# Performance work log

Measured on AMD Instinct MI355X. Metric: run time of the kernel, lower is better.

## Reference

```python
import jax, jax.numpy as jnp
import numpy as np

N_NODES = 51200
N_GRAPHS = 64
NODES_PER_GRAPH = 800
N_EDGES = 819200
DIM_IN = 128
DIM_HIDDEN = 64
HEADS = 3
DIM_OUT = 64


def leaky(x, slope):
    return jnp.where(x >= 0, x, slope * x)


def setup_inputs() -> dict:
    key = jax.random.key(0)
    ks = jax.random.split(key, 12)
    s = lambda fan_in: 1.0 / np.sqrt(fan_in)
    X = jax.random.normal(ks[0], (N_NODES, DIM_IN), dtype=jnp.float32)
    edge_indices = jax.random.randint(ks[1], (2, N_EDGES), 0, N_NODES, dtype=jnp.int32)
    ptr = (jnp.arange(N_GRAPHS + 1, dtype=jnp.int32) * NODES_PER_GRAPH)
    # linearSeq: Linear(dim_in, dim_hidden) + LeakyReLU
    W1 = jax.random.uniform(ks[2], (DIM_IN, DIM_HIDDEN), jnp.float32, -s(DIM_IN), s(DIM_IN))
    b1 = jax.random.uniform(ks[3], (DIM_HIDDEN,), jnp.float32, -s(DIM_IN), s(DIM_IN))
    # GATConv params: lin_src/lin_dst (no bias), att_src/att_dst, bias (concat=False -> out_channels)
    W_src = jax.random.uniform(ks[4], (DIM_HIDDEN, HEADS * DIM_HIDDEN), jnp.float32, -s(DIM_HIDDEN), s(DIM_HIDDEN))
    W_dst = jax.random.uniform(ks[5], (DIM_HIDDEN, HEADS * DIM_HIDDEN), jnp.float32, -s(DIM_HIDDEN), s(DIM_HIDDEN))
    att_src = jax.random.normal(ks[6], (HEADS, DIM_HIDDEN), dtype=jnp.float32) * 0.1
    att_dst = jax.random.normal(ks[7], (HEADS, DIM_HIDDEN), dtype=jnp.float32) * 0.1
    gat_bias = jnp.zeros((DIM_HIDDEN,), dtype=jnp.float32)
    # linear_final: Linear(2*dim_hidden, dim_out)
    Wf = jax.random.uniform(ks[8], (2 * DIM_HIDDEN, DIM_OUT), jnp.float32, -s(2 * DIM_HIDDEN), s(2 * DIM_HIDDEN))
    bf = jax.random.uniform(ks[9], (DIM_OUT,), jnp.float32, -s(2 * DIM_HIDDEN), s(2 * DIM_HIDDEN))
    return {"X": X, "W1": W1, "b1": b1, "W_src": W_src, "W_dst": W_dst,
            "att_src": att_src, "att_dst": att_dst, "gat_bias": gat_bias,
            "Wf": Wf, "bf": bf, "edge_indices": edge_indices, "ptr": ptr}


def reference(X, W1, b1, W_src, W_dst, att_src, att_dst, gat_bias, Wf, bf, edge_indices, ptr):
    N = X.shape[0]
    src, dst = edge_indices[0], edge_indices[1]  # message flows src -> dst
    # input projection
    h = leaky(X @ W1 + b1, 0.01)                                  # [N, DH]
    # GATConv (heads=3, concat=False, add_self_loops=False)
    x_src = (h @ W_src).reshape(N, HEADS, DIM_HIDDEN)             # [N, H, C]
    x_dst = (h @ W_dst).reshape(N, HEADS, DIM_HIDDEN)
    a_src = jnp.einsum('nhc,hc->nh', x_src, att_src)              # [N, H]
    a_dst = jnp.einsum('nhc,hc->nh', x_dst, att_dst)
    logits = leaky(a_src[src] + a_dst[dst], 0.2)                  # [E, H]
    # segment softmax over incoming edges of each target node
    m = jax.ops.segment_max(logits, dst, num_segments=N)          # [N, H]
    e = jnp.exp(logits - m[dst])
    denom = jax.ops.segment_sum(e, dst, num_segments=N)           # [N, H]
    attn = e / denom[dst]                                         # [E, H]
    msg = x_src[src] * attn[..., None]                            # [E, H, C]
    agg = jax.ops.segment_sum(msg, dst, num_segments=N)           # [N, H, C]
    out = agg.mean(axis=1) + gat_bias                             # concat=False -> head mean
    # final head
    cat = jnp.concatenate([h, out], axis=1)                       # [N, 2*DH]
    y = leaky(cat, 0.01) @ Wf + bf                                # [N, DO]
    # aggregate_using_ptr: mean-pool nodes per graph using CSR ptr
    node_graph = jnp.searchsorted(ptr, jnp.arange(N), side='right') - 1
    sums = jax.ops.segment_sum(y, node_graph, num_segments=ptr.shape[0] - 1)
    counts = (ptr[1:] - ptr[:-1]).astype(y.dtype)
    pooled = sums / counts[:, None]                               # [n_graphs, DO]
    return pooled, attn
```

## Files before the change

### kernel.cpp

```cpp
#include <hip/hip_runtime.h>
#include <hip/hip_bf16.h>

#define N_NODES   51200
#define N_GRAPHS  64
#define N_EDGES   819200
#define DIM_IN    128
#define DH        64
#define HEADS     3
#define DIM_OUT   64
#define CAP       96
#define NPART     8
#define PART_SZ   (N_NODES / NPART)

typedef __hip_bfloat16 bf16;
typedef short bf16x8 __attribute__((ext_vector_type(8)));
typedef float f32x4  __attribute__((ext_vector_type(4)));

__device__ __forceinline__ float b2f(bf16 x) { return __bfloat162float(x); }
__device__ __forceinline__ bf16  f2b(float x) { return __float2bfloat16(x); }
__device__ __forceinline__ short f2bs(float x) { return (short)__bfloat16_as_ushort(f2b(x)); }
__device__ __forceinline__ float leaky(float x, float s) { return x >= 0.f ? x : s * x; }
__device__ __forceinline__ float ldin(const void* p, size_t i, int f32) {
    return f32 ? ((const float*)p)[i] : b2f(((const bf16*)p)[i]);
}
__device__ __forceinline__ bf16x8 ld8(const void* p, size_t i, int f32) {
    if (!f32) return *((const bf16x8*)((const short*)p + i));
    const float* f = (const float*)p + i;
    bf16x8 r;
    #pragma unroll
    for (int j = 0; j < 8; ++j) r[j] = f2bs(f[j]);
    return r;
}

__global__ __launch_bounds__(256) void detect_kernel(const unsigned short* __restrict__ Xu,
                                                     int* __restrict__ flag) {
    __shared__ int cnt;
    int tid = threadIdx.x;
    if (tid == 0) cnt = 0;
    __syncthreads();
    int local = 0;
    for (int i = tid * 2; i < 8192; i += 512) {
        unsigned e = (Xu[i] >> 7) & 0xFF;
        if (e >= 110 && e <= 135) local++;
    }
    atomicAdd(&cnt, local);
    __syncthreads();
    if (tid == 0) *flag = (cnt < 2048) ? 1 : 0;
}

__global__ __launch_bounds__(256) void scatter_prep_kernel(const int* __restrict__ src,
                                                           const int* __restrict__ dst,
                                                           int* __restrict__ cursor,
                                                           unsigned short* __restrict__ bucket,
                                                           const void* __restrict__ W1,
                                                           const void* __restrict__ Wsrc,
                                                           const void* __restrict__ Wdst,
                                                           const void* __restrict__ Wf,
                                                           const void* __restrict__ att_src,
                                                           const void* __restrict__ att_dst,
                                                           const int* __restrict__ flagp,
                                                           short* __restrict__ W1t,
                                                           short* __restrict__ Wspt,
                                                           short* __restrict__ Wft,
                                                           short* __restrict__ Wat) {
    if (blockIdx.x < NPART * (N_EDGES / 2048)) {
        const int p = blockIdx.x & (NPART - 1);
        const int slice = blockIdx.x >> 3;
        const int lo = p * PART_SZ, hi = lo + PART_SZ;
        const int base = slice * 2048 + threadIdx.x;
        #pragma unroll
        for (int t = 0; t < 8; ++t) {
            int e = base + t * 256;
            int d = dst[e];
            if (d >= lo && d < hi) {
                int pos = atomicAdd(&cursor[d], 1);
                if (pos < CAP) bucket[(size_t)d * CAP + pos] = (unsigned short)src[e];
            }
        }
        return;
    }
    const int f32 = *flagp;
    int idx = (blockIdx.x - NPART * (N_EDGES / 2048)) * 256 + threadIdx.x;
    if (idx < 8192) {
        int n = idx >> 7, k = idx & 127;
        W1t[idx] = f2bs(ldin(W1, (size_t)k * 64 + n, f32));
    } else if (idx < 20480) {
        int j = idx - 8192;
        int col = j / 192;
        int rem = j - col * 192;
        int h = rem >> 6, kk = rem & 63;
        Wspt[j] = f2bs(ldin(Wsrc, (size_t)kk * 192 + h * 64 + col, f32) * (1.0f / 3.0f));
    } else if (idx < 28672) {
        int j = idx - 20480;
        int n = j >> 7, k = j & 127;
        Wft[j] = f2bs(ldin(Wf, (size_t)k * 64 + n, f32));
    } else if (idx < 29696) {
        int j = idx - 28672;
        int n = j >> 6, k = j & 63;
        float v = 0.f;
        if (n < 3) {
            for (int c = 0; c < 64; ++c)
                v += ldin(Wsrc, (size_t)k * 192 + n * 64 + c, f32) * ldin(att_src, n * 64 + c, f32);
        } else if (n < 6) {
            for (int c = 0; c < 64; ++c)
                v += ldin(Wdst, (size_t)k * 192 + (n - 3) * 64 + c, f32) * ldin(att_dst, (n - 3) * 64 + c, f32);
        }
        Wat[j] = f2bs(v);
    }
}

__global__ __launch_bounds__(256) void k1_kernel(const void* __restrict__ X,
                                                 const short* __restrict__ W1t,
                                                 const short* __restrict__ Wat,
                                                 const void* __restrict__ b1,
                                                 const int* __restrict__ flagp,
                                                 bf16* __restrict__ h_bf,
                                                 float* __restrict__ a_src4,
                                                 float* __restrict__ a_dst4) {
    const int f32 = *flagp;
    __shared__ short hs[64 * 72];
    const int tid  = threadIdx.x;
    const int w    = tid >> 6;
    const int lane = tid & 63;
    const int lm   = lane & 15;
    const int q    = lane >> 4;
    const int row0 = blockIdx.x * 64;

    const float bias = ldin(b1, w * 16 + lm, f32);
    for (int mt = 0; mt < 4; ++mt) {
        f32x4 acc = {0.f, 0.f, 0.f, 0.f};
        #pragma unroll
        for (int kc = 0; kc < 4; ++kc) {
            bf16x8 a = ld8(X, (size_t)(row0 + mt * 16 + lm) * 128 + kc * 32 + q * 8, f32);
            bf16x8 b = *((const bf16x8*)(W1t + (size_t)(w * 16 + lm) * 128 + kc * 32 + q * 8));
            acc = __builtin_amdgcn_mfma_f32_16x16x32_bf16(a, b, acc, 0, 0, 0);
        }
        #pragma unroll
        for (int r = 0; r < 4; ++r) {
            int row = mt * 16 + q * 4 + r;
            float v = leaky(acc[r] + bias, 0.01f);
            short hv = f2bs(v);
            hs[row * 72 + w * 16 + lm] = hv;
            h_bf[(size_t)(row0 + row) * 64 + w * 16 + lm] = __ushort_as_bfloat16((unsigned short)hv);
        }
    }
    __syncthreads();

    {
        const int mt = w;
        bf16x8 a0  = *((const bf16x8*)(hs + (mt * 16 + lm) * 72 + q * 8));
        bf16x8 a1  = *((const bf16x8*)(hs + (mt * 16 + lm) * 72 + 32 + q * 8));
        bf16x8 b0  = *((const bf16x8*)(Wat + (size_t)lm * 64 + q * 8));
        bf16x8 b1v = *((const bf16x8*)(Wat + (size_t)lm * 64 + 32 + q * 8));
        f32x4 acca = {0.f, 0.f, 0.f, 0.f};
        acca = __builtin_amdgcn_mfma_f32_16x16x32_bf16(a0, b0, acca, 0, 0, 0);
        acca = __builtin_amdgcn_mfma_f32_16x16x32_bf16(a1, b1v, acca, 0, 0, 0);
        if (lm < 6) {
            #pragma unroll
            for (int r = 0; r < 4; ++r) {
                int row = row0 + mt * 16 + q * 4 + r;
                if (lm < 3) a_src4[(size_t)row * 4 + lm] = acca[r];
                else        a_dst4[(size_t)row * 4 + (lm - 3)] = acca[r];
            }
        }
    }
}

__global__ __launch_bounds__(256) void edge_kernel(const unsigned short* __restrict__ bucket,
                                                   const int* __restrict__ cursor,
                                                   const float* __restrict__ a_src4,
                                                   const float* __restrict__ a_dst4,
                                                   const unsigned short* __restrict__ hu,
                                                   float4* __restrict__ dstinfo,
                                                   bf16* __restrict__ wagg) {
    const int lane = threadIdx.x & 63;
    const int w = threadIdx.x >> 6;
    const int n = blockIdx.x * 4 + w;
    const int dg = min(cursor[n], CAP);
    const float4 ad = ((const float4*)a_dst4)[n];
    __shared__ float4 buf[4][64];
    float den0 = 0.f, den1 = 0.f, den2 = 0.f;
    float acc0 = 0.f, acc1 = 0.f, acc2 = 0.f;
    for (int c0 = 0; c0 < dg; c0 += 64) {
        int cnt = min(64, dg - c0);
        if (lane < cnt) {
            int s = bucket[n * CAP + c0 + lane];
            const float4 as = ((const float4*)a_src4)[s];
            float e0 = __expf(leaky(as.x + ad.x, 0.2f));
            float e1 = __expf(leaky(as.y + ad.y, 0.2f));
            float e2 = __expf(leaky(as.z + ad.z, 0.2f));
            buf[w][lane] = make_float4(e0, e1, e2, __int_as_float(s));
        }
        asm volatile("s_waitcnt lgkmcnt(0)" ::: "memory");
        int j = 0;
        for (; j + 8 <= cnt; j += 8) {
            float4 r[8]; unsigned short hv[8];
            #pragma unroll
            for (int u = 0; u < 8; ++u) r[u] = buf[w][j + u];
            #pragma unroll
            for (int u = 0; u < 8; ++u)
                hv[u] = hu[(((unsigned)__float_as_int(r[u].w)) << 6) | (unsigned)lane];
            #pragma unroll
            for (int u = 0; u < 8; ++u) {
                float f = b2f(__ushort_as_bfloat16(hv[u]));
                acc0 += r[u].x * f; acc1 += r[u].y * f; acc2 += r[u].z * f;
                den0 += r[u].x;     den1 += r[u].y;     den2 += r[u].z;
            }
        }
        for (; j < cnt; ++j) {
            float4 r = buf[w][j];
            unsigned short hvv = hu[(((unsigned)__float_as_int(r.w)) << 6) | (unsigned)lane];
            float f = b2f(__ushort_as_bfloat16(hvv));
            acc0 += r.x * f; acc1 += r.y * f; acc2 += r.z * f;
            den0 += r.x;     den1 += r.y;     den2 += r.z;
        }
    }
    float inv0 = den0 > 0.f ? 1.f / den0 : 0.f;
    float inv1 = den1 > 0.f ? 1.f / den1 : 0.f;
    float inv2 = den2 > 0.f ? 1.f / den2 : 0.f;
    size_t wb = (size_t)n * 192;
    wagg[wb + lane]       = f2b(acc0 * inv0);
    wagg[wb + 64 + lane]  = f2b(acc1 * inv1);
    wagg[wb + 128 + lane] = f2b(acc2 * inv2);
    if (lane == 0) {
        dstinfo[(size_t)n * 2 + 0] = make_float4(ad.x, ad.y, ad.z, 0.f);
        dstinfo[(size_t)n * 2 + 1] = make_float4(inv0, inv1, inv2, 0.f);
    }
}

__global__ __launch_bounds__(256) void attn_g3_kernel(const int* __restrict__ src,
                                                      const int* __restrict__ dst,
                                                      const float* __restrict__ a_src4,
                                                      const float4* __restrict__ dstinfo,
                                                      const bf16* __restrict__ h_bf,
                                                      const bf16* __restrict__ wagg,
                                                      const short* __restrict__ Wspt,
                                                      const short* __restrict__ Wft,
                                                      const void* __restrict__ gat_bias,
                                                      const void* __restrict__ bfv,
                                                      const int* __restrict__ flagp,
                                                      bf16* __restrict__ y_bf,
                                                      void* __restrict__ d_out) {
    const int f32 = *flagp;
    __shared__ short cs[64 * 136];
    if (blockIdx.x < N_EDGES / 256) {
        int e = blockIdx.x * 256 + threadIdx.x;
        int s = src[e], d = dst[e];
        const float4 as = ((const float4*)a_src4)[s];
        const float4 ad = dstinfo[(size_t)d * 2 + 0];
        const float4 cv = dstinfo[(size_t)d * 2 + 1];
        float a0 = __expf(leaky(as.x + ad.x, 0.2f)) * cv.x;
        float a1 = __expf(leaky(as.y + ad.y, 0.2f)) * cv.y;
        float a2 = __expf(leaky(as.z + ad.z, 0.2f)) * cv.z;
        size_t o = (size_t)N_GRAPHS * DIM_OUT + (size_t)e * 3;
        if (f32) {
            float* p = (float*)d_out;
            p[o] = a0; p[o + 1] = a1; p[o + 2] = a2;
        } else {
            bf16* p = (bf16*)d_out;
            p[o] = f2b(a0); p[o + 1] = f2b(a1); p[o + 2] = f2b(a2);
        }
        return;
    }
    const int bid  = blockIdx.x - N_EDGES / 256;
    const int tid  = threadIdx.x;
    const int w    = tid >> 6;
    const int lane = tid & 63;
    const int lm   = lane & 15;
    const int q    = lane >> 4;
    const int row0 = bid * 64;
    for (int idx = tid; idx < 64 * 64; idx += 256) {
        int r = idx >> 6, k = idx & 63;
        cs[r * 136 + k] = f2bs(leaky(b2f(h_bf[(size_t)(row0 + r) * 64 + k]), 0.01f));
    }
    {
        const int col = w * 16 + lm;
        const float gb = ldin(gat_bias, col, f32);
        for (int mt = 0; mt < 4; ++mt) {
            f32x4 acc = {0.f, 0.f, 0.f, 0.f};
            #pragma unroll
            for (int kc = 0; kc < 6; ++kc) {
                bf16x8 a = *((const bf16x8*)((const short*)wagg + (size_t)(row0 + mt * 16 + lm) * 192 + kc * 32 + q * 8));
                bf16x8 b = *((const bf16x8*)(Wspt + (size_t)col * 192 + kc * 32 + q * 8));
                acc = __builtin_amdgcn_mfma_f32_16x16x32_bf16(a, b, acc, 0, 0, 0);
            }
            #pragma unroll
            for (int r = 0; r < 4; ++r) {
                int row = mt * 16 + q * 4 + r;
                cs[row * 136 + 64 + col] = f2bs(leaky(acc[r] + gb, 0.01f));
            }
        }
    }
    __syncthreads();
    const float bias = ldin(bfv, w * 16 + lm, f32);
    for (int mt = 0; mt < 4; ++mt) {
        f32x4 acc = {0.f, 0.f, 0.f, 0.f};
        #pragma unroll
        for (int kc = 0; kc < 4; ++kc) {
            bf16x8 a = *((const bf16x8*)(cs + (mt * 16 + lm) * 136 + kc * 32 + q * 8));
            bf16x8 b = *((const bf16x8*)(Wft + (size_t)(w * 16 + lm) * 128 + kc * 32 + q * 8));
            acc = __builtin_amdgcn_mfma_f32_16x16x32_bf16(a, b, acc, 0, 0, 0);
        }
        #pragma unroll
        for (int r = 0; r < 4; ++r) {
            int row = row0 + mt * 16 + q * 4 + r;
            y_bf[(size_t)row * 64 + w * 16 + lm] = f2b(acc[r] + bias);
        }
    }
}

__global__ __launch_bounds__(1024) void pool_kernel(const bf16* __restrict__ y_bf,
                                                    const int* __restrict__ ptr,
                                                    const int* __restrict__ flagp,
                                                    void* __restrict__ d_out) {
    __shared__ float part[16][64];
    const int f32 = *flagp;
    const int g = blockIdx.x;
    const int w = threadIdx.x >> 6, lane = threadIdx.x & 63;
    const int lo = ptr[g], hi = ptr[g + 1];
    const int cnt = hi - lo;
    float s = 0.f;
    for (int i = lo + w; i < hi; i += 16) s += b2f(y_bf[(size_t)i * DIM_OUT + lane]);
    part[w][lane] = s;
    __syncthreads();
    if (threadIdx.x < 64) {
        float t = 0.f;
        #pragma unroll
        for (int k = 0; k < 16; ++k) t += part[k][threadIdx.x];
        float v = t / (float)cnt;
        if (f32) ((float*)d_out)[g * DIM_OUT + threadIdx.x] = v;
        else     ((bf16*)d_out)[g * DIM_OUT + threadIdx.x]  = f2b(v);
    }
}

extern "C" void kernel_launch(void* const* d_in, const int* in_sizes, int n_in,
                              void* d_out, int out_size, void* d_ws, size_t ws_size,
                              hipStream_t stream) {
    const void* X        = d_in[0];
    const void* W1       = d_in[1];
    const void* b1       = d_in[2];
    const void* Wsrc     = d_in[3];
    const void* Wdst     = d_in[4];
    const void* att_src  = d_in[5];
    const void* att_dst  = d_in[6];
    const void* gat_bias = d_in[7];
    const void* Wf       = d_in[8];
    const void* bfv      = d_in[9];
    const int*  ei       = (const int*)d_in[10];
    const int*  ptr      = (const int*)d_in[11];
    const int*  src  = ei;
    const int*  dstp = ei + N_EDGES;

    char* ws = (char*)d_ws;
    size_t off_b = 0;
    auto alloc = [&](size_t bytes) -> char* {
        char* p = ws + off_b;
        off_b += (bytes + 255) & ~(size_t)255;
        return p;
    };
    int*     flag    = (int*)    alloc(256);
    short*   W1t     = (short*)  alloc(8192 * 2);
    short*   Wspt    = (short*)  alloc(12288 * 2);
    short*   Wft     = (short*)  alloc(8192 * 2);
    short*   Wat     = (short*)  alloc(1024 * 2);
    bf16*    h_bf    = (bf16*)   alloc((size_t)N_NODES * 64 * 2);
    float*   a_src4  = (float*)  alloc((size_t)N_NODES * 16);
    float*   a_dst4  = (float*)  alloc((size_t)N_NODES * 16);
    float4*  dstinfo = (float4*) alloc((size_t)N_NODES * 2 * 16);
    bf16*    wagg    = (bf16*)   alloc((size_t)N_NODES * 192 * 2);
    int*     cursor  = (int*)    alloc((size_t)N_NODES * 4);
    unsigned short* bucket = (unsigned short*)alloc((size_t)N_NODES * CAP * 2);
    bf16*    y_bf    = (bf16*)   bucket;
    if (off_b > ws_size) return;

    hipLaunchKernelGGL(detect_kernel, dim3(1), dim3(256), 0, stream,
                       (const unsigned short*)X, flag);
    hipMemsetAsync(cursor, 0, (size_t)N_NODES * 4, stream);
    hipLaunchKernelGGL(scatter_prep_kernel,
                       dim3(NPART * (N_EDGES / 2048) + 116), dim3(256), 0, stream,
                       src, dstp, cursor, bucket,
                       W1, Wsrc, Wdst, Wf, att_src, att_dst, flag, W1t, Wspt, Wft, Wat);
    hipLaunchKernelGGL(k1_kernel, dim3(N_NODES / 64), dim3(256), 0, stream,
                       X, W1t, Wat, b1, flag, h_bf, a_src4, a_dst4);
    hipLaunchKernelGGL(edge_kernel, dim3(N_NODES / 4), dim3(256), 0, stream,
                       bucket, cursor, a_src4, a_dst4,
                       (const unsigned short*)h_bf, dstinfo, wagg);
    hipLaunchKernelGGL(attn_g3_kernel, dim3(N_EDGES / 256 + N_NODES / 64), dim3(256), 0, stream,
                       src, dstp, a_src4, dstinfo, h_bf, wagg, Wspt, Wft,
                       gat_bias, bfv, flag, y_bf, d_out);
    hipLaunchKernelGGL(pool_kernel, dim3(N_GRAPHS), dim3(1024), 0, stream, y_bf, ptr, flag, d_out);
}
```

Baseline: 237.5 us.

## Fuse edge scatter with input projection and gather fp8 node features

Splits the weight prep into a small prep kernel for W1/attention vectors, then fuses the edge bucketing scatter, the input projection GEMM, and the remaining weight transposes into a single multi-role kernel so they run concurrently. The projection now also writes an fp8 copy of h, which the edge aggregation kernel gathers instead of bf16 to halve random-gather bytes. The softmax denominator is accumulated once per edge during exp computation and reduced with a wave shuffle instead of being redundantly summed per lane. This trades accuracy of the aggregated messages (fp8 quantisation) for bandwidth, and adds an extra launch plus extra h8 writes.

New measurement: 248.8 us. 1.05x slower.

```diff
diff --git a/kernel.cpp b/kernel.cpp
--- a/kernel.cpp
+++ b/kernel.cpp
@@ -11,6 +11,9 @@
 #define CAP       96
 #define NPART     8
 #define PART_SZ   (N_NODES / NPART)
+#define SC_BLOCKS (NPART * (N_EDGES / 2048))
+#define K1_BLOCKS (N_NODES / 64)
+#define P2_BLOCKS 80
 
 typedef __hip_bfloat16 bf16;
 typedef short bf16x8 __attribute__((ext_vector_type(8)));
@@ -48,54 +51,21 @@
     if (tid == 0) *flag = (cnt < 2048) ? 1 : 0;
 }
 
-__global__ __launch_bounds__(256) void scatter_prep_kernel(const int* __restrict__ src,
-                                                           const int* __restrict__ dst,
-                                                           int* __restrict__ cursor,
-                                                           unsigned short* __restrict__ bucket,
-                                                           const void* __restrict__ W1,
-                                                           const void* __restrict__ Wsrc,
-                                                           const void* __restrict__ Wdst,
-                                                           const void* __restrict__ Wf,
-                                                           const void* __restrict__ att_src,
-                                                           const void* __restrict__ att_dst,
-                                                           const int* __restrict__ flagp,
-                                                           short* __restrict__ W1t,
-                                                           short* __restrict__ Wspt,
-                                                           short* __restrict__ Wft,
-                                                           short* __restrict__ Wat) {
-    if (blockIdx.x < NPART * (N_EDGES / 2048)) {
-        const int p = blockIdx.x & (NPART - 1);
-        const int slice = blockIdx.x >> 3;
-        const int lo = p * PART_SZ, hi = lo + PART_SZ;
-        const int base = slice * 2048 + threadIdx.x;
-        #pragma unroll
-        for (int t = 0; t < 8; ++t) {
-            int e = base + t * 256;
-            int d = dst[e];
-            if (d >= lo && d < hi) {
-                int pos = atomicAdd(&cursor[d], 1);
-                if (pos < CAP) bucket[(size_t)d * CAP + pos] = (unsigned short)src[e];
-            }
-        }
-        return;
-    }
+__global__ __launch_bounds__(256) void prep1_kernel(const void* __restrict__ W1,
+                                                    const void* __restrict__ Wsrc,
+                                                    const void* __restrict__ Wdst,
+                                                    const void* __restrict__ att_src,
+                                                    const void* __restrict__ att_dst,
+                                                    const int* __restrict__ flagp,
+                                                    short* __restrict__ W1t,
+                                                    short* __restrict__ Wat) {
     const int f32 = *flagp;
-    int idx = (blockIdx.x - NPART * (N_EDGES / 2048)) * 256 + threadIdx.x;
+    int idx = blockIdx.x * 256 + threadIdx.x;
     if (idx < 8192) {
         int n = idx >> 7, k = idx & 127;
         W1t[idx] = f2bs(ldin(W1, (size_t)k * 64 + n, f32));
-    } else if (idx < 20480) {
+    } else if (idx < 9216) {
         int j = idx - 8192;
-        int col = j / 192;
-        int rem = j - col * 192;
-        int h = rem >> 6, kk = rem & 63;
-        Wspt[j] = f2bs(ldin(Wsrc, (size_t)kk * 192 + h * 64 + col, f32) * (1.0f / 3.0f));
-    } else if (idx < 28672) {
-        int j = idx - 20480;
-        int n = j >> 7, k = j & 127;
-        Wft[j] = f2bs(ldin(Wf, (size_t)k * 64 + n, f32));
-    } else if (idx < 29696) {
-        int j = idx - 28672;
         int n = j >> 6, k = j & 63;
         float v = 0.f;
         if (n < 3) {
@@ -109,14 +79,54 @@
     }
 }
 
-__global__ __launch_bounds__(256) void k1_kernel(const void* __restrict__ X,
-                                                 const short* __restrict__ W1t,
-                                                 const short* __restrict__ Wat,
-                                                 const void* __restrict__ b1,
-                                                 const int* __restrict__ flagp,
-                                                 bf16* __restrict__ h_bf,
-                                                 float* __restrict__ a_src4,
-                                                 float* __restrict__ a_dst4) {
+__global__ __launch_bounds__(256) void mega_kernel(const int* __restrict__ src,
+                                                   const int* __restrict__ dst,
+                                                   int* __restrict__ cursor,
+                                                   unsigned short* __restrict__ bucket,
+                                                   const void* __restrict__ X,
+                                                   const short* __restrict__ W1t,
+                                                   const short* __restrict__ Wat,
+                                                   const void* __restrict__ b1,
+                                                   const void* __restrict__ Wsrc,
+                                                   const void* __restrict__ Wf,
+                                                   const int* __restrict__ flagp,
+                                                   bf16* __restrict__ h_bf,
+                                                   unsigned char* __restrict__ h8,
+                                                   float* __restrict__ a_src4,
+                                                   float* __restrict__ a_dst4,
+                                                   short* __restrict__ Wspt,
+                                                   short* __restrict__ Wft) {
+    if (blockIdx.x < SC_BLOCKS) {
+        const int p = blockIdx.x & (NPART - 1);
+        const int slice = blockIdx.x >> 3;
+        const int lo = p * PART_SZ, hi = lo + PART_SZ;
+        const int base = slice * 2048 + threadIdx.x;
+        #pragma unroll
+        for (int t = 0; t < 8; ++t) {
+            int e = base + t * 256;
+            int d = dst[e];
+            if (d >= lo && d < hi) {
+                int pos = atomicAdd(&cursor[d], 1);
+                if (pos < CAP) bucket[(size_t)d * CAP + pos] = (unsigned short)src[e];
+            }
+        }
+        return;
+    }
+    if (blockIdx.x >= SC_BLOCKS + K1_BLOCKS) {
+        const int f32 = *flagp;
+        int idx = (blockIdx.x - SC_BLOCKS - K1_BLOCKS) * 256 + threadIdx.x;
+        if (idx < 12288) {
+            int col = idx / 192;
+            int rem = idx - col * 192;
+            int hh = rem >> 6, kk = rem & 63;
+            Wspt[idx] = f2bs(ldin(Wsrc, (size_t)kk * 192 + hh * 64 + col, f32) * (1.0f / 3.0f));
+        } else {
+            int j = idx - 12288;
+            int n = j >> 7, k = j & 127;
+            Wft[j] = f2bs(ldin(Wf, (size_t)k * 64 + n, f32));
+        }
+        return;
+    }
     const int f32 = *flagp;
     __shared__ short hs[64 * 72];
     const int tid  = threadIdx.x;
@@ -124,7 +134,7 @@
     const int lane = tid & 63;
     const int lm   = lane & 15;
     const int q    = lane >> 4;
-    const int row0 = blockIdx.x * 64;
+    const int row0 = (blockIdx.x - SC_BLOCKS) * 64;
 
     const float bias = ldin(b1, w * 16 + lm, f32);
     for (int mt = 0; mt < 4; ++mt) {
@@ -142,6 +152,8 @@
             short hv = f2bs(v);
             hs[row * 72 + w * 16 + lm] = hv;
             h_bf[(size_t)(row0 + row) * 64 + w * 16 + lm] = __ushort_as_bfloat16((unsigned short)hv);
+            h8[(size_t)(row0 + row) * 64 + w * 16 + lm] =
+                (unsigned char)__builtin_amdgcn_cvt_pk_fp8_f32(v, 0.f, 0, false);
         }
     }
     __syncthreads();
@@ -170,7 +182,7 @@
                                                    const int* __restrict__ cursor,
                                                    const float* __restrict__ a_src4,
                                                    const float* __restrict__ a_dst4,
-                                                   const unsigned short* __restrict__ hu,
+                                                   const unsigned char* __restrict__ h8,
                                                    float4* __restrict__ dstinfo,
                                                    bf16* __restrict__ wagg) {
     const int lane = threadIdx.x & 63;
@@ -189,31 +201,36 @@
             float e0 = __expf(leaky(as.x + ad.x, 0.2f));
             float e1 = __expf(leaky(as.y + ad.y, 0.2f));
             float e2 = __expf(leaky(as.z + ad.z, 0.2f));
+            den0 += e0; den1 += e1; den2 += e2;
             buf[w][lane] = make_float4(e0, e1, e2, __int_as_float(s));
         }
         asm volatile("s_waitcnt lgkmcnt(0)" ::: "memory");
         int j = 0;
         for (; j + 8 <= cnt; j += 8) {
-            float4 r[8]; unsigned short hv[8];
+            float4 r[8]; int hv[8];
             #pragma unroll
             for (int u = 0; u < 8; ++u) r[u] = buf[w][j + u];
             #pragma unroll
             for (int u = 0; u < 8; ++u)
-                hv[u] = hu[(((unsigned)__float_as_int(r[u].w)) << 6) | (unsigned)lane];
+                hv[u] = (int)h8[(((unsigned)__float_as_int(r[u].w)) << 6) | (unsigned)lane];
             #pragma unroll
             for (int u = 0; u < 8; ++u) {
-                float f = b2f(__ushort_as_bfloat16(hv[u]));
+                float f = __builtin_amdgcn_cvt_f32_fp8(hv[u], 0);
                 acc0 += r[u].x * f; acc1 += r[u].y * f; acc2 += r[u].z * f;
-                den0 += r[u].x;     den1 += r[u].y;     den2 += r[u].z;
             }
         }
         for (; j < cnt; ++j) {
             float4 r = buf[w][j];
-            unsigned short hvv = hu[(((unsigned)__float_as_int(r.w)) << 6) | (unsigned)lane];
-            float f = b2f(__ushort_as_bfloat16(hvv));
+            int hvv = (int)h8[(((unsigned)__float_as_int(r.w)) << 6) | (unsigned)lane];
+            float f = __builtin_amdgcn_cvt_f32_fp8(hvv, 0);
             acc0 += r.x * f; acc1 += r.y * f; acc2 += r.z * f;
-            den0 += r.x;     den1 += r.y;     den2 += r.z;
-        }
+        }
+    }
+    #pragma unroll
+    for (int off = 32; off >= 1; off >>= 1) {
+        den0 += __shfl_xor(den0, off);
+        den1 += __shfl_xor(den1, off);
+        den2 += __shfl_xor(den2, off);
     }
     float inv0 = den0 > 0.f ? 1.f / den0 : 0.f;
     float inv1 = den1 > 0.f ? 1.f / den1 : 0.f;
@@ -364,6 +381,7 @@
     short*   Wft     = (short*)  alloc(8192 * 2);
     short*   Wat     = (short*)  alloc(1024 * 2);
     bf16*    h_bf    = (bf16*)   alloc((size_t)N_NODES * 64 * 2);
+    unsigned char* h8 = (unsigned char*)alloc((size_t)N_NODES * 64);
     float*   a_src4  = (float*)  alloc((size_t)N_NODES * 16);
     float*   a_dst4  = (float*)  alloc((size_t)N_NODES * 16);
     float4*  dstinfo = (float4*) alloc((size_t)N_NODES * 2 * 16);
@@ -376,15 +394,14 @@
     hipLaunchKernelGGL(detect_kernel, dim3(1), dim3(256), 0, stream,
                        (const unsigned short*)X, flag);
     hipMemsetAsync(cursor, 0, (size_t)N_NODES * 4, stream);
-    hipLaunchKernelGGL(scatter_prep_kernel,
-                       dim3(NPART * (N_EDGES / 2048) + 116), dim3(256), 0, stream,
+    hipLaunchKernelGGL(prep1_kernel, dim3(36), dim3(256), 0, stream,
+                       W1, Wsrc, Wdst, att_src, att_dst, flag, W1t, Wat);
+    hipLaunchKernelGGL(mega_kernel, dim3(SC_BLOCKS + K1_BLOCKS + P2_BLOCKS), dim3(256), 0, stream,
                        src, dstp, cursor, bucket,
-                       W1, Wsrc, Wdst, Wf, att_src, att_dst, flag, W1t, Wspt, Wft, Wat);
-    hipLaunchKernelGGL(k1_kernel, dim3(N_NODES / 64), dim3(256), 0, stream,
-                       X, W1t, Wat, b1, flag, h_bf, a_src4, a_dst4);
+                       X, W1t, Wat, b1, Wsrc, Wf, flag,
+                       h_bf, h8, a_src4, a_dst4, Wspt, Wft);
     hipLaunchKernelGGL(edge_kernel, dim3(N_NODES / 4), dim3(256), 0, stream,
-                       bucket, cursor, a_src4, a_dst4,
-                       (const unsigned short*)h_bf, dstinfo, wagg);
+                       bucket, cursor, a_src4, a_dst4, h8, dstinfo, wagg);
     hipLaunchKernelGGL(attn_g3_kernel, dim3(N_EDGES / 256 + N_NODES / 64), dim3(256), 0, stream,
                        src, dstp, a_src4, dstinfo, h_bf, wagg, Wspt, Wft,
                        gat_bias, bfv, flag, y_bf, d_out);
```
